# Optimization experiments

Measured on AMD Instinct MI355X. Metric: run time of the kernel, lower is better.

## Reference

```python
import jax, jax.numpy as jnp
import numpy as np

H = 768
NUM_LABELS = 16
LN_EPS = 1e-5


def setup_inputs() -> dict:
    key = jax.random.key(0)
    ks = jax.random.split(key, 12)
    L, B = 192, 4
    s = 0.02
    return {
        "h_ner": jax.random.normal(ks[0], (L, B, H), jnp.float32),
        "h_share": jax.random.normal(ks[1], (L, B, H), jnp.float32),
        "mask": jnp.ones((L, B), jnp.float32),
        # n: Linear(2H -> H)
        "Wn": jax.random.normal(ks[2], (H, 2 * H), jnp.float32) * s,
        "bn": jnp.zeros((H,), jnp.float32),
        # hid2hid: Linear(3H -> H)
        "W1": jax.random.normal(ks[3], (H, 3 * H), jnp.float32) * s,
        "b1": jnp.zeros((H,), jnp.float32),
        # LayerNorm(H)
        "gamma": jnp.ones((H,), jnp.float32),
        "beta": jnp.zeros((H,), jnp.float32),
        # hid2tag: Linear(H -> num_labels)
        "Wt": jax.random.normal(ks[4], (NUM_LABELS, H), jnp.float32) * s,
        "bt": jnp.zeros((NUM_LABELS,), jnp.float32),
    }


def reference(h_ner, h_share, mask, Wn, bn, W1, b1, gamma, beta, Wt, bt):
    L, B, Hd = h_ner.shape
    # n(cat(h_share, h_ner)) decomposed: Wn = [Wn_s | Wn_r] over input dim
    Wn_s, Wn_r = Wn[:, :Hd], Wn[:, Hd:]
    g = jnp.tanh(jnp.einsum('lbh,oh->lbo', h_share, Wn_s)
                 + jnp.einsum('lbh,oh->lbo', h_ner, Wn_r) + bn)
    g = jnp.max(g, axis=0)  # [B, H] global max-pool over length

    # hid2hid(cat(st, en, g)) decomposed into three sub-matmuls (same math as concat+GEMM)
    W_st, W_en, W_g = W1[:, :Hd], W1[:, Hd:2 * Hd], W1[:, 2 * Hd:]
    a = jnp.einsum('lbh,oh->lbo', h_ner, W_st)   # start-span term  [L,B,H]
    c = jnp.einsum('lbh,oh->lbo', h_ner, W_en)   # end-span term    [L,B,H]
    d = jnp.einsum('bh,oh->bo', g, W_g)          # global term      [B,H]
    pre = a[:, None, :, :] + c[None, :, :, :] + d[None, None, :, :] + b1  # [L,L,B,H]

    # LayerNorm over H
    mu = jnp.mean(pre, axis=-1, keepdims=True)
    var = jnp.mean(jnp.square(pre - mu), axis=-1, keepdims=True)
    x = (pre - mu) * jax.lax.rsqrt(var + LN_EPS) * gamma + beta

    # dropout is identity in eval mode; ELU then hid2tag + sigmoid
    x = jax.nn.elu(x)
    ner = jax.nn.sigmoid(jnp.einsum('ijbh,oh->ijbo', x, Wt) + bt)  # [L,L,B,num_labels]

    # upper-triangular span mask (end >= start) combined with token mask
    triu = jnp.triu(jnp.ones((L, L), jnp.float32))          # [L,L]
    m = mask[:, None, :] * mask[None, :, :] * triu[:, :, None]  # [L,L,B]
    return ner * m[..., None]
```

## Files before the change

kernel.cpp:

```cpp
#include <hip/hip_runtime.h>
#include <math.h>

#define L_SEQ 192
#define B_SZ  4
#define H_D   768
#define N_LB  16

__global__ __launch_bounds__(256) void g1_gemm(
    const float* __restrict__ h_ner, const float* __restrict__ h_share,
    const float* __restrict__ Wn, const float* __restrict__ bn,
    const float* __restrict__ W1,
    float* __restrict__ P, float* __restrict__ AC)
{
    __shared__ float As[16][68];
    __shared__ float Bs[16][68];

    const int tid = threadIdx.x;
    const int tx = tid & 15;
    const int ty = tid >> 4;
    const int sr = tid >> 2;
    const int sc = (tid & 3) << 2;

    const int bid = blockIdx.x;
    const bool isP = bid < 144;
    int tm, tn;
    if (isP) { tm = bid / 12; tn = bid - tm * 12; }
    else     { int t = bid - 144; tm = t / 24; tn = t - tm * 24; }
    const int m0 = tm * 64, n0 = tn * 64;

    int bro = 0, bco = 0;
    if (!isP) { if (n0 < 768) { bro = n0; bco = 0; } else { bro = n0 - 768; bco = 768; } }

    const int nsteps = isP ? 96 : 48;
    float acc[4][4] = {};

    auto ldA = [&](int kt) -> float4 {
        const bool ph = isP && (kt >= 48);
        const int k0 = (kt - (ph ? 48 : 0)) << 4;
        const float* src = (isP && !ph) ? h_share : h_ner;
        return *(const float4*)&src[(m0 + sr) * H_D + k0 + sc];
    };
    auto ldB = [&](int kt) -> float4 {
        const bool ph = isP && (kt >= 48);
        const int k0 = (kt - (ph ? 48 : 0)) << 4;
        const float* p = isP ? &Wn[(n0 + sr) * 1536 + (ph ? 768 : 0) + k0 + sc]
                             : &W1[(bro + sr) * 2304 + bco + k0 + sc];
        return *(const float4*)p;
    };

    float4 av = ldA(0), bv = ldB(0);
    for (int kt = 0; kt < nsteps; ++kt) {
        __syncthreads();
        As[sc + 0][sr] = av.x; As[sc + 1][sr] = av.y; As[sc + 2][sr] = av.z; As[sc + 3][sr] = av.w;
        Bs[sc + 0][sr] = bv.x; Bs[sc + 1][sr] = bv.y; Bs[sc + 2][sr] = bv.z; Bs[sc + 3][sr] = bv.w;
        __syncthreads();
        if (kt + 1 < nsteps) { av = ldA(kt + 1); bv = ldB(kt + 1); }
        #pragma unroll
        for (int kk = 0; kk < 16; ++kk) {
            const float4 a4 = *(const float4*)&As[kk][ty << 2];
            const float4 b4 = *(const float4*)&Bs[kk][tx << 2];
            const float ar[4] = {a4.x, a4.y, a4.z, a4.w};
            const float bc[4] = {b4.x, b4.y, b4.z, b4.w};
            #pragma unroll
            for (int r = 0; r < 4; ++r)
                #pragma unroll
                for (int c = 0; c < 4; ++c)
                    acc[r][c] = fmaf(ar[r], bc[c], acc[r][c]);
        }
    }

    if (isP) {
        const int o = n0 + (tx << 2);
        const float4 bnv = *(const float4*)&bn[o];
        #pragma unroll
        for (int r = 0; r < 4; ++r) {
            const int m = m0 + (ty << 2) + r;
            float4 v;
            v.x = tanhf(acc[r][0] + bnv.x);
            v.y = tanhf(acc[r][1] + bnv.y);
            v.z = tanhf(acc[r][2] + bnv.z);
            v.w = tanhf(acc[r][3] + bnv.w);
            *(float4*)&P[m * 768 + o] = v;
        }
    } else {
        #pragma unroll
        for (int r = 0; r < 4; ++r) {
            const int m = m0 + (ty << 2) + r;
            float4 v = make_float4(acc[r][0], acc[r][1], acc[r][2], acc[r][3]);
            *(float4*)&AC[m * 1536 + n0 + (tx << 2)] = v;
        }
    }
}

__global__ __launch_bounds__(256) void g2a_gmax(const float* __restrict__ P,
                                                float* __restrict__ g)
{
    const int idx = blockIdx.x * 256 + threadIdx.x;
    const int b = idx / 768;
    const int o = idx - b * 768;
    float m = -1e30f;
    for (int l = 0; l < L_SEQ; ++l)
        m = fmaxf(m, P[l * 3072 + b * 768 + o]);
    g[idx] = m;
}

__global__ __launch_bounds__(256) void g2b_dd(const float* __restrict__ g,
                                              const float* __restrict__ W1,
                                              const float* __restrict__ b1,
                                              float* __restrict__ dd)
{
    const int b = blockIdx.x & 3;
    const int og = blockIdx.x >> 2;
    const int w = threadIdx.x >> 6;
    const int lane = threadIdx.x & 63;
    const int o = og * 4 + w;
    const float* wr = W1 + o * 2304 + 1536;
    const float* gr = g + b * 768;
    float acc = 0.f;
    #pragma unroll
    for (int m = 0; m < 12; ++m) {
        const int h = lane + 64 * m;
        acc = fmaf(gr[h], wr[h], acc);
    }
    #pragma unroll
    for (int mm = 32; mm; mm >>= 1) acc += __shfl_xor(acc, mm, 64);
    if (lane == 0) dd[b * 768 + o] = acc + b1[o];
}

__global__ __launch_bounds__(256) void ep_kernel(
    const float* __restrict__ AC, const float* __restrict__ dd,
    const float* __restrict__ mask,
    const float* __restrict__ gamma, const float* __restrict__ beta,
    const float* __restrict__ Wt, const float* __restrict__ bt,
    float* __restrict__ out)
{
    __shared__ float wt_s[N_LB * H_D];
    __shared__ float rbuf[4][64][16];

    const int tid = threadIdx.x;
    for (int r = tid; r < N_LB * H_D; r += 256) wt_s[r] = Wt[r];

    const int b = blockIdx.x & 3;
    const int x = blockIdx.x >> 2;
    const int w = tid >> 6;
    const int lane = tid & 63;
    const int jgrp = lane >> 4;
    const int tl = lane & 15;
    const float btv = bt[tl];
    const float4* wt4 = (const float4*)wt_s;

    float4 gam[3], bet[3], ddv[3];
    #pragma unroll
    for (int k2 = 0; k2 < 3; ++k2) {
        const int ob = (lane << 2) + (k2 << 8);
        gam[k2] = *(const float4*)&gamma[ob];
        bet[k2] = *(const float4*)&beta[ob];
        ddv[k2] = *(const float4*)&dd[b * 768 + ob];
    }
    __syncthreads();

    #pragma unroll 1
    for (int half = 0; half < 2; ++half) {
        const int i = half ? (191 - x) : x;
        const float mi = mask[i * 4 + b];
        float4 pbase[3];
        {
            const float4* arow = (const float4*)&AC[(i * 4 + b) * 1536];
            #pragma unroll
            for (int k2 = 0; k2 < 3; ++k2) {
                const float4 a4 = arow[lane + (k2 << 6)];
                pbase[k2].x = a4.x + ddv[k2].x;
                pbase[k2].y = a4.y + ddv[k2].y;
                pbase[k2].z = a4.z + ddv[k2].z;
                pbase[k2].w = a4.w + ddv[k2].w;
            }
        }
        #pragma unroll 1
        for (int jt = i + (w << 2); jt < L_SEQ; jt += 16) {
            float4 pre[4][3];
            float s1[4], s2[4];
            #pragma unroll
            for (int jj = 0; jj < 4; ++jj) {
                int j = jt + jj; if (j > 191) j = 191;
                const float4* crow = (const float4*)&AC[(j * 4 + b) * 1536 + 768];
                s1[jj] = 0.f; s2[jj] = 0.f;
                #pragma unroll
                for (int k2 = 0; k2 < 3; ++k2) {
                    const float4 cv = crow[lane + (k2 << 6)];
                    float4 p;
                    p.x = pbase[k2].x + cv.x;
                    p.y = pbase[k2].y + cv.y;
                    p.z = pbase[k2].z + cv.z;
                    p.w = pbase[k2].w + cv.w;
                    pre[jj][k2] = p;
                    s1[jj] += p.x + p.y + p.z + p.w;
                    s2[jj] = fmaf(p.x, p.x, fmaf(p.y, p.y, fmaf(p.z, p.z, fmaf(p.w, p.w, s2[jj]))));
                }
            }
            #pragma unroll
            for (int m = 32; m; m >>= 1) {
                #pragma unroll
                for (int jj = 0; jj < 4; ++jj) {
                    s1[jj] += __shfl_xor(s1[jj], m, 64);
                    s2[jj] += __shfl_xor(s2[jj], m, 64);
                }
            }
            float mu[4], rs[4];
            #pragma unroll
            for (int jj = 0; jj < 4; ++jj) {
                mu[jj] = s1[jj] * (1.0f / 768.0f);
                const float var = s2[jj] * (1.0f / 768.0f) - mu[jj] * mu[jj];
                rs[jj] = 1.0f / sqrtf(var + 1e-5f);
            }
            #pragma unroll
            for (int jj = 0; jj < 4; ++jj)
                #pragma unroll
                for (int k2 = 0; k2 < 3; ++k2) {
                    float4 p = pre[jj][k2];
                    p.x = (p.x - mu[jj]) * rs[jj] * gam[k2].x + bet[k2].x;
                    p.y = (p.y - mu[jj]) * rs[jj] * gam[k2].y + bet[k2].y;
                    p.z = (p.z - mu[jj]) * rs[jj] * gam[k2].z + bet[k2].z;
                    p.w = (p.w - mu[jj]) * rs[jj] * gam[k2].w + bet[k2].w;
                    p.x = p.x > 0.f ? p.x : __expf(p.x) - 1.f;
                    p.y = p.y > 0.f ? p.y : __expf(p.y) - 1.f;
                    p.z = p.z > 0.f ? p.z : __expf(p.z) - 1.f;
                    p.w = p.w > 0.f ? p.w : __expf(p.w) - 1.f;
                    pre[jj][k2] = p;
                }
            float part[4][16];
            #pragma unroll
            for (int jj = 0; jj < 4; ++jj)
                #pragma unroll
                for (int t = 0; t < 16; ++t) part[jj][t] = 0.f;
            #pragma unroll
            for (int k2 = 0; k2 < 3; ++k2) {
                #pragma unroll
                for (int t = 0; t < 16; ++t) {
                    const float4 wv = wt4[t * 192 + lane + (k2 << 6)];
                    #pragma unroll
                    for (int jj = 0; jj < 4; ++jj) {
                        float s = part[jj][t];
                        s = fmaf(pre[jj][k2].x, wv.x, s);
                        s = fmaf(pre[jj][k2].y, wv.y, s);
                        s = fmaf(pre[jj][k2].z, wv.z, s);
                        s = fmaf(pre[jj][k2].w, wv.w, s);
                        part[jj][t] = s;
                    }
                }
            }
            float fin = 0.f;
            #pragma unroll
            for (int jj = 0; jj < 4; ++jj) {
                #pragma unroll
                for (int t = 0; t < 16; ++t)
                    rbuf[w][lane][t ^ tl] = part[jj][t];
                float rs_ = 0.f;
                #pragma unroll
                for (int s = 0; s < 16; ++s)
                    rs_ += rbuf[w][(jgrp << 4) + s][tl ^ s];
                rs_ += __shfl_xor(rs_, 16, 64);
                rs_ += __shfl_xor(rs_, 32, 64);
                if (jgrp == jj) fin = rs_;
            }
            const int j = jt + jgrp;
            if (j < L_SEQ) {
                const float z = fin + btv;
                const float sg = 1.0f / (1.0f + __expf(-z));
                const float mj = mask[j * 4 + b];
                out[((i * L_SEQ + j) * 4 + b) * N_LB + tl] = sg * mi * mj;
            }
        }
    }
}

extern "C" void kernel_launch(void* const* d_in, const int* in_sizes, int n_in,
                              void* d_out, int out_size, void* d_ws, size_t ws_size,
                              hipStream_t stream)
{
    const float* h_ner   = (const float*)d_in[0];
    const float* h_share = (const float*)d_in[1];
    const float* mask    = (const float*)d_in[2];
    const float* Wn      = (const float*)d_in[3];
    const float* bn      = (const float*)d_in[4];
    const float* W1      = (const float*)d_in[5];
    const float* b1      = (const float*)d_in[6];
    const float* gamma   = (const float*)d_in[7];
    const float* beta    = (const float*)d_in[8];
    const float* Wt      = (const float*)d_in[9];
    const float* bt      = (const float*)d_in[10];

    float* P  = (float*)d_ws;
    float* AC = P + 768 * 768;
    float* g  = AC + 768 * 1536;
    float* dd = g + 4 * 768;

    hipMemsetAsync(d_out, 0, (size_t)out_size * sizeof(float), stream);

    hipLaunchKernelGGL(g1_gemm, dim3(432), dim3(256), 0, stream,
                       h_ner, h_share, Wn, bn, W1, P, AC);
    hipLaunchKernelGGL(g2a_gmax, dim3(12), dim3(256), 0, stream, P, g);
    hipLaunchKernelGGL(g2b_dd, dim3(768), dim3(256), 0, stream, g, W1, b1, dd);
    hipLaunchKernelGGL(ep_kernel, dim3(384), dim3(256), 0, stream,
                       AC, dd, mask, gamma, beta, Wt, bt, (float*)d_out);
}
```

Baseline: 284.7 us.

## Split epilogue j-loop across two blocks and reduce labels with shuffle transpose

Doubles the epilogue grid by giving each (i,b) pair two blocks that interleave j-tiles, and sets a launch-bounds occupancy hint of 3 blocks. The LDS-based cross-lane reduction of the 16-label partial sums is replaced by a recursive-halving shuffle transpose, which removes the rbuf shared buffer and its writes and reads. gamma, beta and dd are now loaded inside the loop rather than held in registers across it, to lower register pressure. tanh is moved after the max-pool, which is valid because tanh is monotonic, so it runs on 3072 values instead of the full GEMM output. The costs are a larger 64-float accumulator array per thread and Wt being staged into shared memory twice as many times.

After: 510.4 us. 1.79x slower.

```diff
diff --git a/kernel.cpp b/kernel.cpp
--- a/kernel.cpp
+++ b/kernel.cpp
@@ -8,7 +8,7 @@
 
 __global__ __launch_bounds__(256) void g1_gemm(
     const float* __restrict__ h_ner, const float* __restrict__ h_share,
-    const float* __restrict__ Wn, const float* __restrict__ bn,
+    const float* __restrict__ Wn,
     const float* __restrict__ W1,
     float* __restrict__ P, float* __restrict__ AC)
 {
@@ -70,17 +70,11 @@
     }
 
     if (isP) {
-        const int o = n0 + (tx << 2);
-        const float4 bnv = *(const float4*)&bn[o];
         #pragma unroll
         for (int r = 0; r < 4; ++r) {
             const int m = m0 + (ty << 2) + r;
-            float4 v;
-            v.x = tanhf(acc[r][0] + bnv.x);
-            v.y = tanhf(acc[r][1] + bnv.y);
-            v.z = tanhf(acc[r][2] + bnv.z);
-            v.w = tanhf(acc[r][3] + bnv.w);
-            *(float4*)&P[m * 768 + o] = v;
+            float4 v = make_float4(acc[r][0], acc[r][1], acc[r][2], acc[r][3]);
+            *(float4*)&P[m * 768 + n0 + (tx << 2)] = v;
         }
     } else {
         #pragma unroll
@@ -93,6 +87,7 @@
 }
 
 __global__ __launch_bounds__(256) void g2a_gmax(const float* __restrict__ P,
+                                                const float* __restrict__ bn,
                                                 float* __restrict__ g)
 {
     const int idx = blockIdx.x * 256 + threadIdx.x;
@@ -101,7 +96,7 @@
     float m = -1e30f;
     for (int l = 0; l < L_SEQ; ++l)
         m = fmaxf(m, P[l * 3072 + b * 768 + o]);
-    g[idx] = m;
+    g[idx] = tanhf(bn[o] + m);
 }
 
 __global__ __launch_bounds__(256) void g2b_dd(const float* __restrict__ g,
@@ -127,7 +122,7 @@
     if (lane == 0) dd[b * 768 + o] = acc + b1[o];
 }
 
-__global__ __launch_bounds__(256) void ep_kernel(
+__global__ __launch_bounds__(256, 3) void ep_kernel(
     const float* __restrict__ AC, const float* __restrict__ dd,
     const float* __restrict__ mask,
     const float* __restrict__ gamma, const float* __restrict__ beta,
@@ -135,13 +130,13 @@
     float* __restrict__ out)
 {
     __shared__ float wt_s[N_LB * H_D];
-    __shared__ float rbuf[4][64][16];
 
     const int tid = threadIdx.x;
     for (int r = tid; r < N_LB * H_D; r += 256) wt_s[r] = Wt[r];
 
     const int b = blockIdx.x & 3;
-    const int x = blockIdx.x >> 2;
+    const int s = (blockIdx.x >> 2) & 1;
+    const int x = blockIdx.x >> 3;
     const int w = tid >> 6;
     const int lane = tid & 63;
     const int jgrp = lane >> 4;
@@ -149,14 +144,6 @@
     const float btv = bt[tl];
     const float4* wt4 = (const float4*)wt_s;
 
-    float4 gam[3], bet[3], ddv[3];
-    #pragma unroll
-    for (int k2 = 0; k2 < 3; ++k2) {
-        const int ob = (lane << 2) + (k2 << 8);
-        gam[k2] = *(const float4*)&gamma[ob];
-        bet[k2] = *(const float4*)&beta[ob];
-        ddv[k2] = *(const float4*)&dd[b * 768 + ob];
-    }
     __syncthreads();
 
     #pragma unroll 1
@@ -169,14 +156,15 @@
             #pragma unroll
             for (int k2 = 0; k2 < 3; ++k2) {
                 const float4 a4 = arow[lane + (k2 << 6)];
-                pbase[k2].x = a4.x + ddv[k2].x;
-                pbase[k2].y = a4.y + ddv[k2].y;
-                pbase[k2].z = a4.z + ddv[k2].z;
-                pbase[k2].w = a4.w + ddv[k2].w;
+                const float4 d4 = *(const float4*)&dd[b * 768 + (lane << 2) + (k2 << 8)];
+                pbase[k2].x = a4.x + d4.x;
+                pbase[k2].y = a4.y + d4.y;
+                pbase[k2].z = a4.z + d4.z;
+                pbase[k2].w = a4.w + d4.w;
             }
         }
         #pragma unroll 1
-        for (int jt = i + (w << 2); jt < L_SEQ; jt += 16) {
+        for (int jt = i + (w << 2) + (s << 4); jt < L_SEQ; jt += 32) {
             float4 pre[4][3];
             float s1[4], s2[4];
             #pragma unroll
@@ -213,25 +201,27 @@
                 rs[jj] = 1.0f / sqrtf(var + 1e-5f);
             }
             #pragma unroll
-            for (int jj = 0; jj < 4; ++jj)
-                #pragma unroll
-                for (int k2 = 0; k2 < 3; ++k2) {
+            for (int k2 = 0; k2 < 3; ++k2) {
+                const int ob = (lane << 2) + (k2 << 8);
+                const float4 gm = *(const float4*)&gamma[ob];
+                const float4 bt4 = *(const float4*)&beta[ob];
+                #pragma unroll
+                for (int jj = 0; jj < 4; ++jj) {
                     float4 p = pre[jj][k2];
-                    p.x = (p.x - mu[jj]) * rs[jj] * gam[k2].x + bet[k2].x;
-                    p.y = (p.y - mu[jj]) * rs[jj] * gam[k2].y + bet[k2].y;
-                    p.z = (p.z - mu[jj]) * rs[jj] * gam[k2].z + bet[k2].z;
-                    p.w = (p.w - mu[jj]) * rs[jj] * gam[k2].w + bet[k2].w;
+                    p.x = (p.x - mu[jj]) * rs[jj] * gm.x + bt4.x;
+                    p.y = (p.y - mu[jj]) * rs[jj] * gm.y + bt4.y;
+                    p.z = (p.z - mu[jj]) * rs[jj] * gm.z + bt4.z;
+                    p.w = (p.w - mu[jj]) * rs[jj] * gm.w + bt4.w;
                     p.x = p.x > 0.f ? p.x : __expf(p.x) - 1.f;
                     p.y = p.y > 0.f ? p.y : __expf(p.y) - 1.f;
                     p.z = p.z > 0.f ? p.z : __expf(p.z) - 1.f;
                     p.w = p.w > 0.f ? p.w : __expf(p.w) - 1.f;
                     pre[jj][k2] = p;
                 }
-            float part[4][16];
-            #pragma unroll
-            for (int jj = 0; jj < 4; ++jj)
-                #pragma unroll
-                for (int t = 0; t < 16; ++t) part[jj][t] = 0.f;
+            }
+            float v[64];
+            #pragma unroll
+            for (int q = 0; q < 64; ++q) v[q] = 0.f;
             #pragma unroll
             for (int k2 = 0; k2 < 3; ++k2) {
                 #pragma unroll
@@ -239,28 +229,61 @@
                     const float4 wv = wt4[t * 192 + lane + (k2 << 6)];
                     #pragma unroll
                     for (int jj = 0; jj < 4; ++jj) {
-                        float s = part[jj][t];
-                        s = fmaf(pre[jj][k2].x, wv.x, s);
-                        s = fmaf(pre[jj][k2].y, wv.y, s);
-                        s = fmaf(pre[jj][k2].z, wv.z, s);
-                        s = fmaf(pre[jj][k2].w, wv.w, s);
-                        part[jj][t] = s;
+                        float acc = v[(jj << 4) | t];
+                        acc = fmaf(pre[jj][k2].x, wv.x, acc);
+                        acc = fmaf(pre[jj][k2].y, wv.y, acc);
+                        acc = fmaf(pre[jj][k2].z, wv.z, acc);
+                        acc = fmaf(pre[jj][k2].w, wv.w, acc);
+                        v[(jj << 4) | t] = acc;
                     }
                 }
             }
-            float fin = 0.f;
-            #pragma unroll
-            for (int jj = 0; jj < 4; ++jj) {
-                #pragma unroll
-                for (int t = 0; t < 16; ++t)
-                    rbuf[w][lane][t ^ tl] = part[jj][t];
-                float rs_ = 0.f;
-                #pragma unroll
-                for (int s = 0; s < 16; ++s)
-                    rs_ += rbuf[w][(jgrp << 4) + s][tl ^ s];
-                rs_ += __shfl_xor(rs_, 16, 64);
-                rs_ += __shfl_xor(rs_, 32, 64);
-                if (jgrp == jj) fin = rs_;
+            float r32[32];
+            #pragma unroll
+            for (int m = 0; m < 32; ++m) {
+                const float a = v[m], c = v[m + 32];
+                const float keep = (lane & 32) ? c : a;
+                const float send = (lane & 32) ? a : c;
+                r32[m] = keep + __shfl_xor(send, 32, 64);
+            }
+            float r16[16];
+            #pragma unroll
+            for (int m = 0; m < 16; ++m) {
+                const float a = r32[m], c = r32[m + 16];
+                const float keep = (lane & 16) ? c : a;
+                const float send = (lane & 16) ? a : c;
+                r16[m] = keep + __shfl_xor(send, 16, 64);
+            }
+            float r8[8];
+            #pragma unroll
+            for (int m = 0; m < 8; ++m) {
+                const float a = r16[m], c = r16[m + 8];
+                const float keep = (lane & 8) ? c : a;
+                const float send = (lane & 8) ? a : c;
+                r8[m] = keep + __shfl_xor(send, 8, 64);
+            }
+            float r4[4];
+            #pragma unroll
+            for (int m = 0; m < 4; ++m) {
+                const float a = r8[m], c = r8[m + 4];
+                const float keep = (lane & 4) ? c : a;
+                const float send = (lane & 4) ? a : c;
+                r4[m] = keep + __shfl_xor(send, 4, 64);
+            }
+            float r2[2];
+            #pragma unroll
+            for (int m = 0; m < 2; ++m) {
+                const float a = r4[m], c = r4[m + 2];
+                const float keep = (lane & 2) ? c : a;
+                const float send = (lane & 2) ? a : c;
+                r2[m] = keep + __shfl_xor(send, 2, 64);
+            }
+            float fin;
+            {
+                const float a = r2[0], c = r2[1];
+                const float keep = (lane & 1) ? c : a;
+                const float send = (lane & 1) ? a : c;
+                fin = keep + __shfl_xor(send, 1, 64);
             }
             const int j = jt + jgrp;
             if (j < L_SEQ) {
@@ -297,9 +320,9 @@
     hipMemsetAsync(d_out, 0, (size_t)out_size * sizeof(float), stream);
 
     hipLaunchKernelGGL(g1_gemm, dim3(432), dim3(256), 0, stream,
-                       h_ner, h_share, Wn, bn, W1, P, AC);
-    hipLaunchKernelGGL(g2a_gmax, dim3(12), dim3(256), 0, stream, P, g);
+                       h_ner, h_share, Wn, W1, P, AC);
+    hipLaunchKernelGGL(g2a_gmax, dim3(12), dim3(256), 0, stream, P, bn, g);
     hipLaunchKernelGGL(g2b_dd, dim3(768), dim3(256), 0, stream, g, W1, b1, dd);
-    hipLaunchKernelGGL(ep_kernel, dim3(384), dim3(256), 0, stream,
+    hipLaunchKernelGGL(ep_kernel, dim3(768), dim3(256), 0, stream,
                        AC, dd, mask, gamma, beta, Wt, bt, (float*)d_out);
 }
```
